# Performance work log

Measured on AMD Instinct MI355X. Metric: run time of the kernel, lower is better.

The kernel has to match this reference:

```python
import jax, jax.numpy as jnp
import numpy as np

NH = 8       # attention_maps
DK = 256     # key_dimension
DV = 256     # value_dimension
KS = 3       # kernel_size
PAD = (KS - 1) // 2


def _conv(x, w, b, stride, pad):
    y = jax.lax.conv_general_dilated(
        x, w, (stride, stride), [(pad, pad), (pad, pad)],
        dimension_numbers=('NCHW', 'OIHW', 'NCHW'))
    return y + b[None, :, None, None]


def _rel_to_abs(x):
    # x: (B, M, L, 2L-1) -> (B, M, L, L) via the skewing/padding trick
    B, M, L, _ = x.shape
    x = jnp.pad(x, ((0, 0), (0, 0), (0, 0), (0, 1)))          # (B,M,L,2L)
    x = x.reshape(B, M, 2 * L * L)
    x = jnp.pad(x, ((0, 0), (0, 0), (0, L - 1)))
    x = x.reshape(B, M, L + 1, 2 * L - 1)
    return x[:, :, :L, L - 1:]


def _rel_logits_1d(q, kr, H, W, nh, axis):
    # q: (B, nh, H, W, dkh); kr: (2W-1, dkh)
    B = q.shape[0]
    rl = jnp.einsum('bhxyd,md->bhxym', q, kr)                 # (B,nh,H,W,2W-1)
    rl = rl.reshape(B, nh * H, W, 2 * W - 1)
    rl = _rel_to_abs(rl).reshape(B, nh, H, W, W)
    rl = jnp.broadcast_to(rl[:, :, :, None], (B, nh, H, H, W, W))
    if axis == 'x':
        rl = jnp.transpose(rl, (0, 1, 2, 4, 3, 5))
    else:
        # faithful to original torch code (incl. its no-op transpose bug):
        # transpose(4,5) then transpose(3,5) == permutation (0,1,2,4,5,3)
        rl = jnp.transpose(rl, (0, 1, 2, 4, 5, 3))
    return rl.reshape(B, nh, H * W, H * W)


def setup_inputs() -> dict:
    key = jax.random.key(0)
    ks = jax.random.split(key, 10)
    B, Cin, H, W = 4, 128, 32, 32
    Cout = 512
    dkh = DK // NH
    sc = 0.05
    return {
        'x': jax.random.normal(ks[0], (B, Cin, H, W), jnp.float32),
        'conv_w': jax.random.normal(ks[1], (Cout - DV, Cin, KS, KS), jnp.float32) * sc,
        'conv_b': jax.random.normal(ks[2], (Cout - DV,), jnp.float32) * sc,
        'qkv_w': jax.random.normal(ks[3], (2 * DK + DV, Cin, KS, KS), jnp.float32) * sc,
        'qkv_b': jax.random.normal(ks[4], (2 * DK + DV,), jnp.float32) * sc,
        'att_w': jax.random.normal(ks[5], (DV, DV, 1, 1), jnp.float32) * sc,
        'att_b': jax.random.normal(ks[6], (DV,), jnp.float32) * sc,
        'kr_x': jax.random.normal(ks[7], (2 * W - 1, dkh), jnp.float32),
        'kr_y': jax.random.normal(ks[8], (2 * H - 1, dkh), jnp.float32),
    }


def reference(x, conv_w, conv_b, qkv_w, qkv_b, att_w, att_b, kr_x, kr_y):
    B = x.shape[0]
    conv_out = _conv(x, conv_w, conv_b, 1, PAD)               # (B, Cout-DV, H, W)
    H, W = conv_out.shape[2], conv_out.shape[3]
    dkh, dvh = DK // NH, DV // NH

    qkv = _conv(x, qkv_w, qkv_b, 1, PAD)                      # (B, 2DK+DV, H, W)
    q, k, v = jnp.split(qkv, [DK, 2 * DK], axis=1)
    q = q.reshape(B, NH, dkh, H, W) * (dkh ** -0.5)
    k = k.reshape(B, NH, dkh, H, W)
    v = v.reshape(B, NH, dvh, H, W)

    fq = q.reshape(B, NH, dkh, H * W)
    fk = k.reshape(B, NH, dkh, H * W)
    fv = v.reshape(B, NH, dvh, H * W)

    logits = jnp.einsum('bhdi,bhdj->bhij', fq, fk)            # (B,NH,HW,HW)

    # relative logits (scaled q, matching torch which scales before this)
    q_t = jnp.transpose(q, (0, 1, 3, 4, 2))                   # (B,NH,H,W,dkh)
    rel_x = _rel_logits_1d(q_t, kr_x, H, W, NH, 'x')
    rel_y = _rel_logits_1d(jnp.transpose(q_t, (0, 1, 3, 2, 4)), kr_y, W, H, NH, 'y')
    logits = logits + rel_y + rel_x

    weights = jax.nn.softmax(logits, axis=-1)
    att = jnp.einsum('bhij,bhdj->bhid', weights, fv)          # (B,NH,HW,dvh)
    # faithful raw reshape as in torch (no transpose before reshape)
    att = att.reshape(B, NH, dvh, H, W).reshape(B, DV, H, W)
    att = _conv(att, att_w, att_b, 1, 0)
    return jnp.concatenate([conv_out, att], axis=1)
```

## Files before the change

kernel.cpp:

```cpp
#include <hip/hip_runtime.h>
#include <hip/hip_bf16.h>
#include <math.h>

#define BN 4
#define CIN 128
#define HH 32
#define WW 32
#define HWP 1024
#define NHEAD 8

typedef __attribute__((ext_vector_type(8))) short s8v;
typedef __attribute__((ext_vector_type(4))) float f32x4;

__global__ __launch_bounds__(256) void prep_all(
    const float* __restrict__ x,
    const float* __restrict__ conv_w, const float* __restrict__ qkv_w,
    const float* __restrict__ att_w,
    const float* __restrict__ kr_x, const float* __restrict__ kr_y,
    __hip_bfloat16* __restrict__ xT, __hip_bfloat16* __restrict__ Wb,
    __hip_bfloat16* __restrict__ Wab, __hip_bfloat16* __restrict__ krb)
{
    const int bid = blockIdx.x;
    const int tid = threadIdx.x;

    if (bid < 4608) {
        int g = bid * 256 + tid;
        int co = g / 1152;
        int k = g - co * 1152;
        int kk = k >> 7, ci = k & 127;
        float v;
        if (co < 256) v = conv_w[((size_t)(co * 128 + ci) * 9) + kk];
        else          v = qkv_w[((size_t)((co - 256) * 128 + ci) * 9) + kk];
        Wb[(size_t)co * 1152 + k] = __float2bfloat16(v);
    } else if (bid < 4744) {
        __shared__ float xs[CIN][33];
        int rel = bid - 4608;
        int yy = rel >> 2;
        int b = rel & 3;
        const bool inner = (yy >= 1 && yy <= 32);
        if (inner) {
            for (int idx = tid; idx < CIN * 32; idx += 256) {
                int ci = idx >> 5, xx = idx & 31;
                xs[ci][xx] = x[((size_t)(b * CIN + ci) * HH + (yy - 1)) * WW + xx];
            }
        }
        __syncthreads();
        for (int idx = tid; idx < 34 * 128; idx += 256) {
            int xx = idx >> 7, ci = idx & 127;
            float v = 0.f;
            if (inner && xx >= 1 && xx <= 32) v = xs[ci][xx - 1];
            xT[((size_t)(b * 34 + yy) * 34 + xx) * 128 + ci] = __float2bfloat16(v);
        }
    } else if (bid < 5000) {
        int g = (bid - 4744) * 256 + tid;
        Wab[g] = __float2bfloat16(att_w[g]);
    } else {
        for (int idx = tid; idx < 2 * 64 * 32; idx += 256) {
            int axis = idx >> 11;
            int col = (idx >> 5) & 63;
            int d = idx & 31;
            float v = 0.f;
            if (col < 63) v = axis ? kr_y[col * 32 + d] : kr_x[col * 32 + d];
            krb[idx] = __float2bfloat16(v);
        }
    }
}

__global__ __launch_bounds__(256) void conv_gemm(
    const __hip_bfloat16* __restrict__ Wb, const __hip_bfloat16* __restrict__ xT,
    const float* __restrict__ conv_b, const float* __restrict__ qkv_b,
    float* __restrict__ out,
    __hip_bfloat16* __restrict__ qbf, __hip_bfloat16* __restrict__ kbf,
    __hip_bfloat16* __restrict__ vtb)
{
    __shared__ __align__(16) __hip_bfloat16 As[128 * 128];
    __shared__ __align__(16) __hip_bfloat16 Bs[128 * 128];

    const int tid = threadIdx.x;
    const int wv = tid >> 6;
    const int lane = tid & 63;
    const int n16 = lane & 15;
    const int quad = lane >> 4;
    const int co0 = blockIdx.x * 128;
    const int y0 = blockIdx.y * 4;
    const int b = blockIdx.z;
    const int mh = wv >> 1, nh = wv & 1;

    const int rbase = tid >> 4;
    const int hh = tid & 15;
    const int swz = (hh ^ rbase) * 8;
    const __hip_bfloat16* aGbase = Wb + (size_t)(co0 + rbase) * 1152 + hh * 8;

    f32x4 acc[4][4];
#pragma unroll
    for (int i = 0; i < 4; ++i)
#pragma unroll
        for (int j = 0; j < 4; ++j) acc[i][j] = (f32x4){0.f, 0.f, 0.f, 0.f};

    s8v ra[8], rb[8];

    auto load_tile = [&](int kk, s8v* la, s8v* lb) {
        const int ky = kk / 3, kx = kk - ky * 3;
#pragma unroll
        for (int i = 0; i < 8; ++i)
            la[i] = *reinterpret_cast<const s8v*>(aGbase + (size_t)(16 * i) * 1152 + kk * 128);
#pragma unroll
        for (int i = 0; i < 8; ++i) {
            int p = rbase + 16 * i;
            int row = y0 + (p >> 5) + ky;
            int xx = (p & 31) + kx;
            lb[i] = *reinterpret_cast<const s8v*>(
                xT + ((size_t)(b * 34 + row) * 34 + xx) * 128 + hh * 8);
        }
    };

    load_tile(0, ra, rb);

    for (int s = 0; s < 9; ++s) {
        __syncthreads();
#pragma unroll
        for (int i = 0; i < 8; ++i) {
            *reinterpret_cast<s8v*>(&As[(rbase + 16 * i) * 128 + swz]) = ra[i];
            *reinterpret_cast<s8v*>(&Bs[(rbase + 16 * i) * 128 + swz]) = rb[i];
        }
        __syncthreads();
        if (s < 8) load_tile(s + 1, ra, rb);

#pragma unroll
        for (int ksub = 0; ksub < 4; ++ksub) {
            const int chunk = ((ksub * 4 + quad) ^ n16) * 8;
            s8v af[4], bfr[4];
#pragma unroll
            for (int mt = 0; mt < 4; ++mt)
                af[mt] = *reinterpret_cast<const s8v*>(&As[(mh * 64 + mt * 16 + n16) * 128 + chunk]);
#pragma unroll
            for (int nt = 0; nt < 4; ++nt)
                bfr[nt] = *reinterpret_cast<const s8v*>(&Bs[(nh * 64 + nt * 16 + n16) * 128 + chunk]);
#pragma unroll
            for (int mt = 0; mt < 4; ++mt)
#pragma unroll
                for (int nt = 0; nt < 4; ++nt)
                    acc[mt][nt] = __builtin_amdgcn_mfma_f32_16x16x32_bf16(af[mt], bfr[nt], acc[mt][nt], 0, 0, 0);
        }
    }

    const int coBase = co0 + mh * 64;
    const int pixBase = y0 * 32 + nh * 64;
    const int seg = coBase >> 8;

    if (seg == 0) {
#pragma unroll
        for (int mt = 0; mt < 4; ++mt)
#pragma unroll
            for (int r = 0; r < 4; ++r) {
                int co = coBase + mt * 16 + quad * 4 + r;
                float bias = conv_b[co];
                float* op = out + (size_t)(b * 512 + co) * HWP + pixBase;
#pragma unroll
                for (int nt = 0; nt < 4; ++nt)
                    op[nt * 16 + n16] = acc[mt][nt][r] + bias;
            }
    } else if (seg == 1) {
        const float scale = 0.17677669529663687f;
#pragma unroll
        for (int mt = 0; mt < 4; ++mt)
#pragma unroll
            for (int r = 0; r < 4; ++r) {
                int c2 = coBase - 256 + mt * 16 + quad * 4 + r;
                float bias = qkv_b[c2];
                int h = c2 >> 5, d = c2 & 31;
                int bh = b * NHEAD + h;
#pragma unroll
                for (int nt = 0; nt < 4; ++nt) {
                    int pix = pixBase + nt * 16 + n16;
                    qbf[((size_t)bh * HWP + pix) * 32 + d] =
                        __float2bfloat16((acc[mt][nt][r] + bias) * scale);
                }
            }
    } else if (seg == 2) {
#pragma unroll
        for (int mt = 0; mt < 4; ++mt)
#pragma unroll
            for (int r = 0; r < 4; ++r) {
                int c2 = coBase - 512 + mt * 16 + quad * 4 + r;
                float bias = qkv_b[c2 + 256];
                int h = c2 >> 5, d = c2 & 31;
                int bh = b * NHEAD + h;
#pragma unroll
                for (int nt = 0; nt < 4; ++nt) {
                    int pix = pixBase + nt * 16 + n16;
                    kbf[((size_t)bh * HWP + pix) * 32 + d] =
                        __float2bfloat16(acc[mt][nt][r] + bias);
                }
            }
    } else {
#pragma unroll
        for (int mt = 0; mt < 4; ++mt)
#pragma unroll
            for (int r = 0; r < 4; ++r) {
                int c2 = coBase - 768 + mt * 16 + quad * 4 + r;
                float bias = qkv_b[c2 + 512];
                int h = c2 >> 5, d = c2 & 31;
                int bh = b * NHEAD + h;
                __hip_bfloat16* vp = vtb + ((size_t)bh * 32 + d) * HWP + pixBase;
#pragma unroll
                for (int nt = 0; nt < 4; ++nt)
                    vp[nt * 16 + n16] = __float2bfloat16(acc[mt][nt][r] + bias);
            }
    }
}

__global__ __launch_bounds__(256) void attn_kernel(
    const __hip_bfloat16* __restrict__ qbf, const __hip_bfloat16* __restrict__ kbf,
    const __hip_bfloat16* __restrict__ vtb, const __hip_bfloat16* __restrict__ krb,
    __hip_bfloat16* __restrict__ attc)
{
    __shared__ __align__(16) float QrX[4][16][68];
    __shared__ __align__(16) float QrY[4][16][68];
    __shared__ __align__(16) __hip_bfloat16 Pb[4][16][40];

    const int tid = threadIdx.x;
    const int wv = tid >> 6;
    const int lane = tid & 63;
    const int n16 = lane & 15;
    const int quad = lane >> 4;
    const int bh = blockIdx.x;
    const int i0 = (blockIdx.y * 4 + wv) * 16;
    const int xi0 = i0 & 31;
    const int yi0 = i0 >> 5;

    s8v aq = *reinterpret_cast<const s8v*>(
        qbf + ((size_t)bh * HWP + i0 + n16) * 32 + quad * 8);
    s8v aqT = *reinterpret_cast<const s8v*>(
        qbf + ((size_t)bh * HWP + (xi0 + n16) * 32 + yi0) * 32 + quad * 8);

#pragma unroll
    for (int t = 0; t < 4; ++t) {
        s8v bx = *reinterpret_cast<const s8v*>(krb + ((size_t)(t * 16 + n16)) * 32 + quad * 8);
        s8v by = *reinterpret_cast<const s8v*>(krb + ((size_t)(64 + t * 16 + n16)) * 32 + quad * 8);
        f32x4 cx = {0.f, 0.f, 0.f, 0.f}, cy = {0.f, 0.f, 0.f, 0.f};
        cx = __builtin_amdgcn_mfma_f32_16x16x32_bf16(aq, bx, cx, 0, 0, 0);
        cy = __builtin_amdgcn_mfma_f32_16x16x32_bf16(aqT, by, cy, 0, 0, 0);
#pragma unroll
        for (int r = 0; r < 4; ++r) {
            QrX[wv][quad * 4 + r][t * 16 + n16] = cx[r];
            QrY[wv][quad * 4 + r][t * 16 + n16] = cy[r];
        }
    }

    float rx0[4], rx1[4];
    int rybase[4];
#pragma unroll
    for (int r = 0; r < 4; ++r) {
        int xi = xi0 + quad * 4 + r;
        rx0[r] = QrX[wv][quad * 4 + r][n16 + 31 - xi];
        rx1[r] = QrX[wv][quad * 4 + r][n16 + 47 - xi];
        rybase[r] = 31 - xi;
    }

    float lsum[4] = {0.f, 0.f, 0.f, 0.f};
    f32x4 O0 = {0.f, 0.f, 0.f, 0.f}, O1 = {0.f, 0.f, 0.f, 0.f};

    const __hip_bfloat16* kbase = kbf + (size_t)bh * HWP * 32;
    const __hip_bfloat16* vbase = vtb + (size_t)bh * 32 * HWP;

    s8v bk0 = *reinterpret_cast<const s8v*>(kbase + ((size_t)n16 * 32 + quad * 8));
    s8v bk1 = *reinterpret_cast<const s8v*>(kbase + ((size_t)(16 + n16) * 32 + quad * 8));
    s8v bv0 = *reinterpret_cast<const s8v*>(vbase + ((size_t)n16 * HWP + quad * 8));
    s8v bv1 = *reinterpret_cast<const s8v*>(vbase + ((size_t)(n16 + 16) * HWP + quad * 8));

    for (int jt = 0; jt < 32; ++jt) {
        s8v cbk0 = bk0, cbk1 = bk1, cbv0 = bv0, cbv1 = bv1;
        if (jt < 31) {
            const int jn = (jt + 1) * 32;
            bk0 = *reinterpret_cast<const s8v*>(kbase + ((size_t)(jn + n16) * 32 + quad * 8));
            bk1 = *reinterpret_cast<const s8v*>(kbase + ((size_t)(jn + 16 + n16) * 32 + quad * 8));
            bv0 = *reinterpret_cast<const s8v*>(vbase + ((size_t)n16 * HWP + jn + quad * 8));
            bv1 = *reinterpret_cast<const s8v*>(vbase + ((size_t)(n16 + 16) * HWP + jn + quad * 8));
        }

        f32x4 s0 = {0.f, 0.f, 0.f, 0.f}, s1 = {0.f, 0.f, 0.f, 0.f};
        s0 = __builtin_amdgcn_mfma_f32_16x16x32_bf16(aq, cbk0, s0, 0, 0, 0);
        s1 = __builtin_amdgcn_mfma_f32_16x16x32_bf16(aq, cbk1, s1, 0, 0, 0);

#pragma unroll
        for (int r = 0; r < 4; ++r) {
            float ryv = QrY[wv][quad * 4 + r][jt + rybase[r]];
            float p0 = __expf(s0[r] + rx0[r] + ryv);
            float p1 = __expf(s1[r] + rx1[r] + ryv);
            lsum[r] += p0 + p1;
            Pb[wv][quad * 4 + r][n16]      = __float2bfloat16(p0);
            Pb[wv][quad * 4 + r][n16 + 16] = __float2bfloat16(p1);
        }
        s8v pA = *reinterpret_cast<const s8v*>(&Pb[wv][n16][quad * 8]);
        O0 = __builtin_amdgcn_mfma_f32_16x16x32_bf16(pA, cbv0, O0, 0, 0, 0);
        O1 = __builtin_amdgcn_mfma_f32_16x16x32_bf16(pA, cbv1, O1, 0, 0, 0);
    }

    const int b = bh >> 3, h = bh & 7;
#pragma unroll
    for (int r = 0; r < 4; ++r) {
        float l = lsum[r];
        l += __shfl_xor(l, 1);
        l += __shfl_xor(l, 2);
        l += __shfl_xor(l, 4);
        l += __shfl_xor(l, 8);
        float inv = 1.0f / l;
        int i = i0 + quad * 4 + r;
        int yi = i >> 5, xi = i & 31;
        __hip_bfloat16* op = attc + ((size_t)(b * 256 + h * 32 + yi) * 32 + xi) * 32;
        op[n16] = __float2bfloat16(O0[r] * inv);
        op[n16 + 16] = __float2bfloat16(O1[r] * inv);
    }
}

__global__ __launch_bounds__(256) void conv1x1_gemm(
    const __hip_bfloat16* __restrict__ Wab, const __hip_bfloat16* __restrict__ attc,
    const float* __restrict__ att_b, float* __restrict__ out)
{
    __shared__ __align__(16) __hip_bfloat16 Ls[64][264];

    const int tid = threadIdx.x;
    const int wv = tid >> 6;
    const int lane = tid & 63;
    const int n16 = lane & 15;
    const int quad = lane >> 4;
    const int o0 = blockIdx.x * 64;
    const int p0 = blockIdx.y * 64;
    const int b = blockIdx.z;
    const int oW = o0 + (wv >> 1) * 32;
    const int pL = (wv & 1) * 32;

#pragma unroll
    for (int pass = 0; pass < 8; ++pass) {
        int ch = pass * 32 + (tid >> 3);
        int pg = (tid & 7) * 8;
        s8v v = *reinterpret_cast<const s8v*>(
            attc + ((size_t)(b * 256 + ch) * HWP) + p0 + pg);
#pragma unroll
        for (int j = 0; j < 8; ++j)
            Ls[pg + j][ch] = ((const __hip_bfloat16*)&v)[j];
    }
    __syncthreads();

    f32x4 acc[2][2];
#pragma unroll
    for (int i = 0; i < 2; ++i)
#pragma unroll
        for (int j = 0; j < 2; ++j) acc[i][j] = (f32x4){0.f, 0.f, 0.f, 0.f};

#pragma unroll
    for (int ks = 0; ks < 8; ++ks) {
        const int c0 = ks * 32 + quad * 8;
        s8v a0 = *reinterpret_cast<const s8v*>(Wab + (size_t)(oW + n16) * 256 + c0);
        s8v a1 = *reinterpret_cast<const s8v*>(Wab + (size_t)(oW + 16 + n16) * 256 + c0);
        s8v b0 = *reinterpret_cast<const s8v*>(&Ls[pL + n16][c0]);
        s8v b1 = *reinterpret_cast<const s8v*>(&Ls[pL + 16 + n16][c0]);
        acc[0][0] = __builtin_amdgcn_mfma_f32_16x16x32_bf16(a0, b0, acc[0][0], 0, 0, 0);
        acc[0][1] = __builtin_amdgcn_mfma_f32_16x16x32_bf16(a0, b1, acc[0][1], 0, 0, 0);
        acc[1][0] = __builtin_amdgcn_mfma_f32_16x16x32_bf16(a1, b0, acc[1][0], 0, 0, 0);
        acc[1][1] = __builtin_amdgcn_mfma_f32_16x16x32_bf16(a1, b1, acc[1][1], 0, 0, 0);
    }

#pragma unroll
    for (int mt = 0; mt < 2; ++mt)
#pragma unroll
        for (int r = 0; r < 4; ++r) {
            int o = oW + mt * 16 + quad * 4 + r;
            float bias = att_b[o];
            float* op = out + ((size_t)(b * 512 + 256 + o)) * HWP;
#pragma unroll
            for (int nt = 0; nt < 2; ++nt)
                op[p0 + pL + nt * 16 + n16] = acc[mt][nt][r] + bias;
        }
}

extern "C" void kernel_launch(void* const* d_in, const int* in_sizes, int n_in,
                              void* d_out, int out_size, void* d_ws, size_t ws_size,
                              hipStream_t stream) {
    const float* x      = (const float*)d_in[0];
    const float* conv_w = (const float*)d_in[1];
    const float* conv_b = (const float*)d_in[2];
    const float* qkv_w  = (const float*)d_in[3];
    const float* qkv_b  = (const float*)d_in[4];
    const float* att_w  = (const float*)d_in[5];
    const float* att_b  = (const float*)d_in[6];
    const float* kr_x   = (const float*)d_in[7];
    const float* kr_y   = (const float*)d_in[8];
    float* out = (float*)d_out;

    char* base = (char*)d_ws;
    const size_t MB = 1u << 20;
    __hip_bfloat16* qbf  = (__hip_bfloat16*)(base + 0 * MB);
    __hip_bfloat16* kbf  = (__hip_bfloat16*)(base + 2 * MB);
    __hip_bfloat16* vtb  = (__hip_bfloat16*)(base + 4 * MB);
    __hip_bfloat16* xT   = (__hip_bfloat16*)(base + 6 * MB);
    __hip_bfloat16* Wb   = (__hip_bfloat16*)(base + 8 * MB);
    __hip_bfloat16* attc = (__hip_bfloat16*)(base + 11 * MB);
    __hip_bfloat16* Wab  = (__hip_bfloat16*)(base + 13 * MB);
    __hip_bfloat16* krb  = (__hip_bfloat16*)(base + 14 * MB);

    prep_all<<<dim3(5001), 256, 0, stream>>>(
        x, conv_w, qkv_w, att_w, kr_x, kr_y, xT, Wb, Wab, krb);
    conv_gemm<<<dim3(8, 8, 4), 256, 0, stream>>>(
        Wb, xT, conv_b, qkv_b, out, qbf, kbf, vtb);
    attn_kernel<<<dim3(32, 16), 256, 0, stream>>>(qbf, kbf, vtb, krb, attc);
    conv1x1_gemm<<<dim3(4, 16, 4), 256, 0, stream>>>(Wab, attc, att_b, out);
}
```

Measured before the change: 140.1 us.

## Split attention key range across two wave groups with LDS reduction

Doubles the attention block to 512 threads so that each 16-row query tile is handled by two waves, each covering half of the key/value sequence. The upper waves write their partial output accumulators and row sums into shared memory, and after a barrier the lower waves add them in, normalize and store. This shortens the serial key loop per wave and raises the number of waves in flight. In exchange it adds shared memory, one block-wide sync and duplicated relative-logit setup work in both waves.

```diff
diff --git a/kernel.cpp b/kernel.cpp
--- a/kernel.cpp
+++ b/kernel.cpp
@@ -210,22 +210,25 @@
     }
 }
 
-__global__ __launch_bounds__(256) void attn_kernel(
+__global__ __launch_bounds__(512, 4) void attn_kernel(
     const __hip_bfloat16* __restrict__ qbf, const __hip_bfloat16* __restrict__ kbf,
     const __hip_bfloat16* __restrict__ vtb, const __hip_bfloat16* __restrict__ krb,
     __hip_bfloat16* __restrict__ attc)
 {
     __shared__ __align__(16) float QrX[4][16][68];
     __shared__ __align__(16) float QrY[4][16][68];
-    __shared__ __align__(16) __hip_bfloat16 Pb[4][16][40];
+    __shared__ __align__(16) __hip_bfloat16 Pb[8][16][40];
+    __shared__ float Ored[4][64][13];
 
     const int tid = threadIdx.x;
     const int wv = tid >> 6;
     const int lane = tid & 63;
     const int n16 = lane & 15;
     const int quad = lane >> 4;
+    const int itl = wv & 3;
+    const int jh = wv >> 2;
     const int bh = blockIdx.x;
-    const int i0 = (blockIdx.y * 4 + wv) * 16;
+    const int i0 = (blockIdx.y * 4 + itl) * 16;
     const int xi0 = i0 & 31;
     const int yi0 = i0 >> 5;
 
@@ -243,8 +246,8 @@
         cy = __builtin_amdgcn_mfma_f32_16x16x32_bf16(aqT, by, cy, 0, 0, 0);
 #pragma unroll
         for (int r = 0; r < 4; ++r) {
-            QrX[wv][quad * 4 + r][t * 16 + n16] = cx[r];
-            QrY[wv][quad * 4 + r][t * 16 + n16] = cy[r];
+            QrX[itl][quad * 4 + r][t * 16 + n16] = cx[r];
+            QrY[itl][quad * 4 + r][t * 16 + n16] = cy[r];
         }
     }
 
@@ -253,8 +256,8 @@
 #pragma unroll
     for (int r = 0; r < 4; ++r) {
         int xi = xi0 + quad * 4 + r;
-        rx0[r] = QrX[wv][quad * 4 + r][n16 + 31 - xi];
-        rx1[r] = QrX[wv][quad * 4 + r][n16 + 47 - xi];
+        rx0[r] = QrX[itl][quad * 4 + r][n16 + 31 - xi];
+        rx1[r] = QrX[itl][quad * 4 + r][n16 + 47 - xi];
         rybase[r] = 31 - xi;
     }
 
@@ -264,53 +267,77 @@
     const __hip_bfloat16* kbase = kbf + (size_t)bh * HWP * 32;
     const __hip_bfloat16* vbase = vtb + (size_t)bh * 32 * HWP;
 
-    s8v bk0 = *reinterpret_cast<const s8v*>(kbase + ((size_t)n16 * 32 + quad * 8));
-    s8v bk1 = *reinterpret_cast<const s8v*>(kbase + ((size_t)(16 + n16) * 32 + quad * 8));
-    s8v bv0 = *reinterpret_cast<const s8v*>(vbase + ((size_t)n16 * HWP + quad * 8));
-    s8v bv1 = *reinterpret_cast<const s8v*>(vbase + ((size_t)(n16 + 16) * HWP + quad * 8));
-
-    for (int jt = 0; jt < 32; ++jt) {
-        s8v cbk0 = bk0, cbk1 = bk1, cbv0 = bv0, cbv1 = bv1;
-        if (jt < 31) {
-            const int jn = (jt + 1) * 32;
-            bk0 = *reinterpret_cast<const s8v*>(kbase + ((size_t)(jn + n16) * 32 + quad * 8));
-            bk1 = *reinterpret_cast<const s8v*>(kbase + ((size_t)(jn + 16 + n16) * 32 + quad * 8));
-            bv0 = *reinterpret_cast<const s8v*>(vbase + ((size_t)n16 * HWP + jn + quad * 8));
-            bv1 = *reinterpret_cast<const s8v*>(vbase + ((size_t)(n16 + 16) * HWP + jn + quad * 8));
-        }
-
-        f32x4 s0 = {0.f, 0.f, 0.f, 0.f}, s1 = {0.f, 0.f, 0.f, 0.f};
-        s0 = __builtin_amdgcn_mfma_f32_16x16x32_bf16(aq, cbk0, s0, 0, 0, 0);
-        s1 = __builtin_amdgcn_mfma_f32_16x16x32_bf16(aq, cbk1, s1, 0, 0, 0);
-
+    const int jbeg = jh * 16;
+    {
+        const int j0 = jbeg * 32;
+        s8v bk0 = *reinterpret_cast<const s8v*>(kbase + ((size_t)(j0 + n16) * 32 + quad * 8));
+        s8v bk1 = *reinterpret_cast<const s8v*>(kbase + ((size_t)(j0 + 16 + n16) * 32 + quad * 8));
+        s8v bv0 = *reinterpret_cast<const s8v*>(vbase + ((size_t)n16 * HWP + j0 + quad * 8));
+        s8v bv1 = *reinterpret_cast<const s8v*>(vbase + ((size_t)(n16 + 16) * HWP + j0 + quad * 8));
+
+        for (int t = 0; t < 16; ++t) {
+            const int jt = jbeg + t;
+            s8v cbk0 = bk0, cbk1 = bk1, cbv0 = bv0, cbv1 = bv1;
+            if (t < 15) {
+                const int jn = (jt + 1) * 32;
+                bk0 = *reinterpret_cast<const s8v*>(kbase + ((size_t)(jn + n16) * 32 + quad * 8));
+                bk1 = *reinterpret_cast<const s8v*>(kbase + ((size_t)(jn + 16 + n16) * 32 + quad * 8));
+                bv0 = *reinterpret_cast<const s8v*>(vbase + ((size_t)n16 * HWP + jn + quad * 8));
+                bv1 = *reinterpret_cast<const s8v*>(vbase + ((size_t)(n16 + 16) * HWP + jn + quad * 8));
+            }
+
+            f32x4 s0 = {0.f, 0.f, 0.f, 0.f}, s1 = {0.f, 0.f, 0.f, 0.f};
+            s0 = __builtin_amdgcn_mfma_f32_16x16x32_bf16(aq, cbk0, s0, 0, 0, 0);
+            s1 = __builtin_amdgcn_mfma_f32_16x16x32_bf16(aq, cbk1, s1, 0, 0, 0);
+
+#pragma unroll
+            for (int r = 0; r < 4; ++r) {
+                float ryv = QrY[itl][quad * 4 + r][jt + rybase[r]];
+                float p0 = __expf(s0[r] + rx0[r] + ryv);
+                float p1 = __expf(s1[r] + rx1[r] + ryv);
+                lsum[r] += p0 + p1;
+                Pb[wv][quad * 4 + r][n16]      = __float2bfloat16(p0);
+                Pb[wv][quad * 4 + r][n16 + 16] = __float2bfloat16(p1);
+            }
+            s8v pA = *reinterpret_cast<const s8v*>(&Pb[wv][n16][quad * 8]);
+            O0 = __builtin_amdgcn_mfma_f32_16x16x32_bf16(pA, cbv0, O0, 0, 0, 0);
+            O1 = __builtin_amdgcn_mfma_f32_16x16x32_bf16(pA, cbv1, O1, 0, 0, 0);
+        }
+    }
+
+    if (wv >= 4) {
+        float* dst = &Ored[itl][lane][0];
 #pragma unroll
         for (int r = 0; r < 4; ++r) {
-            float ryv = QrY[wv][quad * 4 + r][jt + rybase[r]];
-            float p0 = __expf(s0[r] + rx0[r] + ryv);
-            float p1 = __expf(s1[r] + rx1[r] + ryv);
-            lsum[r] += p0 + p1;
-            Pb[wv][quad * 4 + r][n16]      = __float2bfloat16(p0);
-            Pb[wv][quad * 4 + r][n16 + 16] = __float2bfloat16(p1);
-        }
-        s8v pA = *reinterpret_cast<const s8v*>(&Pb[wv][n16][quad * 8]);
-        O0 = __builtin_amdgcn_mfma_f32_16x16x32_bf16(pA, cbv0, O0, 0, 0, 0);
-        O1 = __builtin_amdgcn_mfma_f32_16x16x32_bf16(pA, cbv1, O1, 0, 0, 0);
-    }
-
-    const int b = bh >> 3, h = bh & 7;
-#pragma unroll
-    for (int r = 0; r < 4; ++r) {
-        float l = lsum[r];
-        l += __shfl_xor(l, 1);
-        l += __shfl_xor(l, 2);
-        l += __shfl_xor(l, 4);
-        l += __shfl_xor(l, 8);
-        float inv = 1.0f / l;
-        int i = i0 + quad * 4 + r;
-        int yi = i >> 5, xi = i & 31;
-        __hip_bfloat16* op = attc + ((size_t)(b * 256 + h * 32 + yi) * 32 + xi) * 32;
-        op[n16] = __float2bfloat16(O0[r] * inv);
-        op[n16 + 16] = __float2bfloat16(O1[r] * inv);
+            dst[r] = O0[r];
+            dst[4 + r] = O1[r];
+            dst[8 + r] = lsum[r];
+        }
+    }
+    __syncthreads();
+    if (wv < 4) {
+        const float* src = &Ored[itl][lane][0];
+#pragma unroll
+        for (int r = 0; r < 4; ++r) {
+            O0[r] += src[r];
+            O1[r] += src[4 + r];
+            lsum[r] += src[8 + r];
+        }
+        const int b = bh >> 3, h = bh & 7;
+#pragma unroll
+        for (int r = 0; r < 4; ++r) {
+            float l = lsum[r];
+            l += __shfl_xor(l, 1);
+            l += __shfl_xor(l, 2);
+            l += __shfl_xor(l, 4);
+            l += __shfl_xor(l, 8);
+            float inv = 1.0f / l;
+            int i = i0 + quad * 4 + r;
+            int yi = i >> 5, xi = i & 31;
+            __hip_bfloat16* op = attc + ((size_t)(b * 256 + h * 32 + yi) * 32 + xi) * 32;
+            op[n16] = __float2bfloat16(O0[r] * inv);
+            op[n16 + 16] = __float2bfloat16(O1[r] * inv);
+        }
     }
 }
 
@@ -404,6 +431,6 @@
         x, conv_w, qkv_w, att_w, kr_x, kr_y, xT, Wb, Wab, krb);
     conv_gemm<<<dim3(8, 8, 4), 256, 0, stream>>>(
         Wb, xT, conv_b, qkv_b, out, qbf, kbf, vtb);
-    attn_kernel<<<dim3(32, 16), 256, 0, stream>>>(qbf, kbf, vtb, krb, attc);
+    attn_kernel<<<dim3(32, 16), 512, 0, stream>>>(qbf, kbf, vtb, krb, attc);
     conv1x1_gemm<<<dim3(4, 16, 4), 256, 0, stream>>>(Wab, attc, att_b, out);
 }
```

Result: no change. 142.2 us (+1.5%).

## Fuse all four stages into one persistent kernel with grid barriers

Applied to the files above, without the earlier changes.

Replaces the four separate launches (prep, conv GEMM, attention, 1x1 conv) with a single persistent kernel of 512 blocks. The stages are separated by atomic-counter grid barriers, and a memset resets the counters before the launch. The aim is to remove launch gaps and tail effects between stages. To fit the fixed grid, the conv GEMM and 1x1 tiles are halved, the prep work becomes a grid-stride loop, and the xT transpose no longer goes through shared memory. This relies on all 512 blocks being co-resident (launch bounds allow 2 per CU) to avoid deadlock, and the smaller tiles reduce data reuse.

```diff
diff --git a/kernel.cpp b/kernel.cpp
--- a/kernel.cpp
+++ b/kernel.cpp
@@ -2,377 +2,367 @@
 #include <hip/hip_bf16.h>
 #include <math.h>
 
-#define BN 4
-#define CIN 128
-#define HH 32
-#define WW 32
 #define HWP 1024
 #define NHEAD 8
+#define NBLK 512
 
 typedef __attribute__((ext_vector_type(8))) short s8v;
 typedef __attribute__((ext_vector_type(4))) float f32x4;
 
-__global__ __launch_bounds__(256) void prep_all(
+#define WB_N   1179648
+#define XT_N   591872
+#define WAB_N  65536
+#define KRB_N  4096
+#define TOT_PREP (WB_N + XT_N + WAB_N + KRB_N)
+
+__device__ __forceinline__ void grid_barrier(unsigned* cnt) {
+    __syncthreads();
+    if (threadIdx.x == 0) {
+        __threadfence();
+        atomicAdd(cnt, 1u);
+        while (atomicAdd(cnt, 0u) < NBLK) __builtin_amdgcn_s_sleep(2);
+        __threadfence();
+    }
+    __syncthreads();
+}
+
+__global__ __launch_bounds__(256, 2) void mega_kernel(
     const float* __restrict__ x,
-    const float* __restrict__ conv_w, const float* __restrict__ qkv_w,
-    const float* __restrict__ att_w,
+    const float* __restrict__ conv_w, const float* __restrict__ conv_b,
+    const float* __restrict__ qkv_w, const float* __restrict__ qkv_b,
+    const float* __restrict__ att_w, const float* __restrict__ att_b,
     const float* __restrict__ kr_x, const float* __restrict__ kr_y,
-    __hip_bfloat16* __restrict__ xT, __hip_bfloat16* __restrict__ Wb,
-    __hip_bfloat16* __restrict__ Wab, __hip_bfloat16* __restrict__ krb)
-{
-    const int bid = blockIdx.x;
-    const int tid = threadIdx.x;
-
-    if (bid < 4608) {
-        int g = bid * 256 + tid;
-        int co = g / 1152;
-        int k = g - co * 1152;
-        int kk = k >> 7, ci = k & 127;
-        float v;
-        if (co < 256) v = conv_w[((size_t)(co * 128 + ci) * 9) + kk];
-        else          v = qkv_w[((size_t)((co - 256) * 128 + ci) * 9) + kk];
-        Wb[(size_t)co * 1152 + k] = __float2bfloat16(v);
-    } else if (bid < 4744) {
-        __shared__ float xs[CIN][33];
-        int rel = bid - 4608;
-        int yy = rel >> 2;
-        int b = rel & 3;
-        const bool inner = (yy >= 1 && yy <= 32);
-        if (inner) {
-            for (int idx = tid; idx < CIN * 32; idx += 256) {
-                int ci = idx >> 5, xx = idx & 31;
-                xs[ci][xx] = x[((size_t)(b * CIN + ci) * HH + (yy - 1)) * WW + xx];
-            }
-        }
-        __syncthreads();
-        for (int idx = tid; idx < 34 * 128; idx += 256) {
-            int xx = idx >> 7, ci = idx & 127;
-            float v = 0.f;
-            if (inner && xx >= 1 && xx <= 32) v = xs[ci][xx - 1];
-            xT[((size_t)(b * 34 + yy) * 34 + xx) * 128 + ci] = __float2bfloat16(v);
-        }
-    } else if (bid < 5000) {
-        int g = (bid - 4744) * 256 + tid;
-        Wab[g] = __float2bfloat16(att_w[g]);
-    } else {
-        for (int idx = tid; idx < 2 * 64 * 32; idx += 256) {
-            int axis = idx >> 11;
-            int col = (idx >> 5) & 63;
-            int d = idx & 31;
-            float v = 0.f;
-            if (col < 63) v = axis ? kr_y[col * 32 + d] : kr_x[col * 32 + d];
-            krb[idx] = __float2bfloat16(v);
-        }
-    }
-}
-
-__global__ __launch_bounds__(256) void conv_gemm(
-    const __hip_bfloat16* __restrict__ Wb, const __hip_bfloat16* __restrict__ xT,
-    const float* __restrict__ conv_b, const float* __restrict__ qkv_b,
     float* __restrict__ out,
     __hip_bfloat16* __restrict__ qbf, __hip_bfloat16* __restrict__ kbf,
-    __hip_bfloat16* __restrict__ vtb)
+    __hip_bfloat16* __restrict__ vtb, __hip_bfloat16* __restrict__ xT,
+    __hip_bfloat16* __restrict__ Wb, __hip_bfloat16* __restrict__ Wab,
+    __hip_bfloat16* __restrict__ krb, __hip_bfloat16* __restrict__ attc,
+    unsigned* __restrict__ bar)
 {
-    __shared__ __align__(16) __hip_bfloat16 As[128 * 128];
-    __shared__ __align__(16) __hip_bfloat16 Bs[128 * 128];
-
+    __shared__ __align__(16) char smem[49152];
+
+    const int bid = blockIdx.x;
     const int tid = threadIdx.x;
     const int wv = tid >> 6;
     const int lane = tid & 63;
     const int n16 = lane & 15;
     const int quad = lane >> 4;
-    const int co0 = blockIdx.x * 128;
-    const int y0 = blockIdx.y * 4;
-    const int b = blockIdx.z;
-    const int mh = wv >> 1, nh = wv & 1;
-
-    const int rbase = tid >> 4;
-    const int hh = tid & 15;
-    const int swz = (hh ^ rbase) * 8;
-    const __hip_bfloat16* aGbase = Wb + (size_t)(co0 + rbase) * 1152 + hh * 8;
-
-    f32x4 acc[4][4];
-#pragma unroll
-    for (int i = 0; i < 4; ++i)
-#pragma unroll
-        for (int j = 0; j < 4; ++j) acc[i][j] = (f32x4){0.f, 0.f, 0.f, 0.f};
-
-    s8v ra[8], rb[8];
-
-    auto load_tile = [&](int kk, s8v* la, s8v* lb) {
-        const int ky = kk / 3, kx = kk - ky * 3;
-#pragma unroll
-        for (int i = 0; i < 8; ++i)
-            la[i] = *reinterpret_cast<const s8v*>(aGbase + (size_t)(16 * i) * 1152 + kk * 128);
-#pragma unroll
-        for (int i = 0; i < 8; ++i) {
-            int p = rbase + 16 * i;
-            int row = y0 + (p >> 5) + ky;
-            int xx = (p & 31) + kx;
-            lb[i] = *reinterpret_cast<const s8v*>(
-                xT + ((size_t)(b * 34 + row) * 34 + xx) * 128 + hh * 8);
-        }
-    };
-
-    load_tile(0, ra, rb);
-
-    for (int s = 0; s < 9; ++s) {
+
+    {
+        for (int g = bid * 256 + tid; g < TOT_PREP; g += NBLK * 256) {
+            if (g < WB_N) {
+                int co = g / 1152;
+                int k = g - co * 1152;
+                int kk = k >> 7, ci = k & 127;
+                float v;
+                if (co < 256) v = conv_w[((size_t)(co * 128 + ci) * 9) + kk];
+                else          v = qkv_w[((size_t)((co - 256) * 128 + ci) * 9) + kk];
+                Wb[(size_t)co * 1152 + k] = __float2bfloat16(v);
+            } else if (g < WB_N + XT_N) {
+                int rel = g - WB_N;
+                int ci = rel & 127;
+                int t = rel >> 7;
+                int xx = t % 34;
+                int t2 = t / 34;
+                int yy = t2 % 34;
+                int b = t2 / 34;
+                float v = 0.f;
+                int gy = yy - 1, gx = xx - 1;
+                if ((unsigned)gy < 32u && (unsigned)gx < 32u)
+                    v = x[((size_t)(b * 128 + ci) * 32 + gy) * 32 + gx];
+                xT[(size_t)rel] = __float2bfloat16(v);
+            } else if (g < WB_N + XT_N + WAB_N) {
+                int rel = g - (WB_N + XT_N);
+                Wab[rel] = __float2bfloat16(att_w[rel]);
+            } else {
+                int rel = g - (WB_N + XT_N + WAB_N);
+                int col = (rel >> 5) & 63;
+                int d = rel & 31;
+                int axis = rel >> 11;
+                float v = 0.f;
+                if (col < 63) v = axis ? kr_y[col * 32 + d] : kr_x[col * 32 + d];
+                krb[rel] = __float2bfloat16(v);
+            }
+        }
+    }
+    grid_barrier(&bar[0]);
+
+    {
+        __hip_bfloat16* As = (__hip_bfloat16*)smem;
+        __hip_bfloat16* Bs = (__hip_bfloat16*)(smem + 32768);
+        const int ph = bid & 1;
+        const int b = (bid >> 1) & 3;
+        const int yt = (bid >> 3) & 7;
+        const int ct = bid >> 6;
+        const int co0 = ct * 128;
+        const int pixBase = yt * 128 + ph * 64;
+        const int row0 = pixBase >> 5;
+        const int mh = wv >> 1, nh = wv & 1;
+        const int rbase = tid >> 4;
+        const int hh = tid & 15;
+        const int swz = (hh ^ rbase) * 8;
+        const __hip_bfloat16* aGbase = Wb + (size_t)(co0 + rbase) * 1152 + hh * 8;
+
+        f32x4 acc[4][2];
+#pragma unroll
+        for (int i = 0; i < 4; ++i)
+#pragma unroll
+            for (int j = 0; j < 2; ++j) acc[i][j] = (f32x4){0.f, 0.f, 0.f, 0.f};
+
+        s8v ra[8], rb2[4];
+        auto load_tile = [&](int kk, s8v* la, s8v* lb) {
+            const int ky = kk / 3, kx = kk - ky * 3;
+#pragma unroll
+            for (int i = 0; i < 8; ++i)
+                la[i] = *reinterpret_cast<const s8v*>(aGbase + (size_t)(16 * i) * 1152 + kk * 128);
+#pragma unroll
+            for (int i = 0; i < 4; ++i) {
+                int p = rbase + 16 * i;
+                lb[i] = *reinterpret_cast<const s8v*>(
+                    xT + ((size_t)(b * 34 + row0 + (p >> 5) + ky) * 34 + (p & 31) + kx) * 128 + hh * 8);
+            }
+        };
+
+        load_tile(0, ra, rb2);
+
+        for (int s = 0; s < 9; ++s) {
+            __syncthreads();
+#pragma unroll
+            for (int i = 0; i < 8; ++i)
+                *reinterpret_cast<s8v*>(&As[(rbase + 16 * i) * 128 + swz]) = ra[i];
+#pragma unroll
+            for (int i = 0; i < 4; ++i)
+                *reinterpret_cast<s8v*>(&Bs[(rbase + 16 * i) * 128 + swz]) = rb2[i];
+            __syncthreads();
+            if (s < 8) load_tile(s + 1, ra, rb2);
+
+#pragma unroll
+            for (int ksub = 0; ksub < 4; ++ksub) {
+                const int chunk = ((ksub * 4 + quad) ^ n16) * 8;
+                s8v af[4], bfr[2];
+#pragma unroll
+                for (int mt = 0; mt < 4; ++mt)
+                    af[mt] = *reinterpret_cast<const s8v*>(&As[(mh * 64 + mt * 16 + n16) * 128 + chunk]);
+#pragma unroll
+                for (int nt = 0; nt < 2; ++nt)
+                    bfr[nt] = *reinterpret_cast<const s8v*>(&Bs[(nh * 32 + nt * 16 + n16) * 128 + chunk]);
+#pragma unroll
+                for (int mt = 0; mt < 4; ++mt)
+#pragma unroll
+                    for (int nt = 0; nt < 2; ++nt)
+                        acc[mt][nt] = __builtin_amdgcn_mfma_f32_16x16x32_bf16(af[mt], bfr[nt], acc[mt][nt], 0, 0, 0);
+            }
+        }
+
+        const int coBase = co0 + mh * 64;
+        const int pixW = pixBase + nh * 32;
+        const int seg = coBase >> 8;
+
+        if (seg == 0) {
+#pragma unroll
+            for (int mt = 0; mt < 4; ++mt)
+#pragma unroll
+                for (int r = 0; r < 4; ++r) {
+                    int co = coBase + mt * 16 + quad * 4 + r;
+                    float bias = conv_b[co];
+                    float* op = out + (size_t)(b * 512 + co) * HWP + pixW;
+#pragma unroll
+                    for (int nt = 0; nt < 2; ++nt)
+                        op[nt * 16 + n16] = acc[mt][nt][r] + bias;
+                }
+        } else if (seg == 1) {
+            const float scale = 0.17677669529663687f;
+#pragma unroll
+            for (int mt = 0; mt < 4; ++mt)
+#pragma unroll
+                for (int r = 0; r < 4; ++r) {
+                    int c2 = coBase - 256 + mt * 16 + quad * 4 + r;
+                    float bias = qkv_b[c2];
+                    int h = c2 >> 5, d = c2 & 31;
+                    int bh = b * NHEAD + h;
+#pragma unroll
+                    for (int nt = 0; nt < 2; ++nt) {
+                        int pix = pixW + nt * 16 + n16;
+                        qbf[((size_t)bh * HWP + pix) * 32 + d] =
+                            __float2bfloat16((acc[mt][nt][r] + bias) * scale);
+                    }
+                }
+        } else if (seg == 2) {
+#pragma unroll
+            for (int mt = 0; mt < 4; ++mt)
+#pragma unroll
+                for (int r = 0; r < 4; ++r) {
+                    int c2 = coBase - 512 + mt * 16 + quad * 4 + r;
+                    float bias = qkv_b[c2 + 256];
+                    int h = c2 >> 5, d = c2 & 31;
+                    int bh = b * NHEAD + h;
+#pragma unroll
+                    for (int nt = 0; nt < 2; ++nt) {
+                        int pix = pixW + nt * 16 + n16;
+                        kbf[((size_t)bh * HWP + pix) * 32 + d] =
+                            __float2bfloat16(acc[mt][nt][r] + bias);
+                    }
+                }
+        } else {
+#pragma unroll
+            for (int mt = 0; mt < 4; ++mt)
+#pragma unroll
+                for (int r = 0; r < 4; ++r) {
+                    int c2 = coBase - 768 + mt * 16 + quad * 4 + r;
+                    float bias = qkv_b[c2 + 512];
+                    int h = c2 >> 5, d = c2 & 31;
+                    int bh = b * NHEAD + h;
+                    __hip_bfloat16* vp = vtb + ((size_t)bh * 32 + d) * HWP + pixW;
+#pragma unroll
+                    for (int nt = 0; nt < 2; ++nt)
+                        vp[nt * 16 + n16] = __float2bfloat16(acc[mt][nt][r] + bias);
+                }
+        }
+    }
+    grid_barrier(&bar[32]);
+
+    {
+        float* QrX = (float*)smem;
+        float* QrY = (float*)(smem + 17408);
+        __hip_bfloat16* Pb = (__hip_bfloat16*)(smem + 34816);
+
+        const int bh = bid & 31;
+        const int iblk = bid >> 5;
+        const int i0 = (iblk * 4 + wv) * 16;
+        const int xi0 = i0 & 31;
+        const int yi0 = i0 >> 5;
+
+        s8v aq = *reinterpret_cast<const s8v*>(
+            qbf + ((size_t)bh * HWP + i0 + n16) * 32 + quad * 8);
+        s8v aqT = *reinterpret_cast<const s8v*>(
+            qbf + ((size_t)bh * HWP + (xi0 + n16) * 32 + yi0) * 32 + quad * 8);
+
+#pragma unroll
+        for (int t = 0; t < 4; ++t) {
+            s8v bx = *reinterpret_cast<const s8v*>(krb + ((size_t)(t * 16 + n16)) * 32 + quad * 8);
+            s8v by = *reinterpret_cast<const s8v*>(krb + ((size_t)(64 + t * 16 + n16)) * 32 + quad * 8);
+            f32x4 cx = {0.f, 0.f, 0.f, 0.f}, cy = {0.f, 0.f, 0.f, 0.f};
+            cx = __builtin_amdgcn_mfma_f32_16x16x32_bf16(aq, bx, cx, 0, 0, 0);
+            cy = __builtin_amdgcn_mfma_f32_16x16x32_bf16(aqT, by, cy, 0, 0, 0);
+#pragma unroll
+            for (int r = 0; r < 4; ++r) {
+                QrX[(wv * 16 + quad * 4 + r) * 68 + t * 16 + n16] = cx[r];
+                QrY[(wv * 16 + quad * 4 + r) * 68 + t * 16 + n16] = cy[r];
+            }
+        }
+
+        float rx0[4], rx1[4];
+        int rybase[4];
+#pragma unroll
+        for (int r = 0; r < 4; ++r) {
+            int xi = xi0 + quad * 4 + r;
+            rx0[r] = QrX[(wv * 16 + quad * 4 + r) * 68 + n16 + 31 - xi];
+            rx1[r] = QrX[(wv * 16 + quad * 4 + r) * 68 + n16 + 47 - xi];
+            rybase[r] = 31 - xi;
+        }
+
+        float lsum[4] = {0.f, 0.f, 0.f, 0.f};
+        f32x4 O0 = {0.f, 0.f, 0.f, 0.f}, O1 = {0.f, 0.f, 0.f, 0.f};
+
+        const __hip_bfloat16* kbase = kbf + (size_t)bh * HWP * 32;
+        const __hip_bfloat16* vbase = vtb + (size_t)bh * 32 * HWP;
+
+        s8v bk0 = *reinterpret_cast<const s8v*>(kbase + ((size_t)n16 * 32 + quad * 8));
+        s8v bk1 = *reinterpret_cast<const s8v*>(kbase + ((size_t)(16 + n16) * 32 + quad * 8));
+        s8v bv0 = *reinterpret_cast<const s8v*>(vbase + ((size_t)n16 * HWP + quad * 8));
+        s8v bv1 = *reinterpret_cast<const s8v*>(vbase + ((size_t)(n16 + 16) * HWP + quad * 8));
+
+        for (int jt = 0; jt < 32; ++jt) {
+            s8v cbk0 = bk0, cbk1 = bk1, cbv0 = bv0, cbv1 = bv1;
+            if (jt < 31) {
+                const int jn = (jt + 1) * 32;
+                bk0 = *reinterpret_cast<const s8v*>(kbase + ((size_t)(jn + n16) * 32 + quad * 8));
+                bk1 = *reinterpret_cast<const s8v*>(kbase + ((size_t)(jn + 16 + n16) * 32 + quad * 8));
+                bv0 = *reinterpret_cast<const s8v*>(vbase + ((size_t)n16 * HWP + jn + quad * 8));
+                bv1 = *reinterpret_cast<const s8v*>(vbase + ((size_t)(n16 + 16) * HWP + jn + quad * 8));
+            }
+
+            f32x4 s0 = {0.f, 0.f, 0.f, 0.f}, s1 = {0.f, 0.f, 0.f, 0.f};
+            s0 = __builtin_amdgcn_mfma_f32_16x16x32_bf16(aq, cbk0, s0, 0, 0, 0);
+            s1 = __builtin_amdgcn_mfma_f32_16x16x32_bf16(aq, cbk1, s1, 0, 0, 0);
+
+#pragma unroll
+            for (int r = 0; r < 4; ++r) {
+                float ryv = QrY[(wv * 16 + quad * 4 + r) * 68 + jt + rybase[r]];
+                float p0 = __expf(s0[r] + rx0[r] + ryv);
+                float p1 = __expf(s1[r] + rx1[r] + ryv);
+                lsum[r] += p0 + p1;
+                Pb[(wv * 16 + quad * 4 + r) * 40 + n16]      = __float2bfloat16(p0);
+                Pb[(wv * 16 + quad * 4 + r) * 40 + n16 + 16] = __float2bfloat16(p1);
+            }
+            s8v pA = *reinterpret_cast<const s8v*>(&Pb[(wv * 16 + n16) * 40 + quad * 8]);
+            O0 = __builtin_amdgcn_mfma_f32_16x16x32_bf16(pA, cbv0, O0, 0, 0, 0);
+            O1 = __builtin_amdgcn_mfma_f32_16x16x32_bf16(pA, cbv1, O1, 0, 0, 0);
+        }
+
+        const int b = bh >> 3, h = bh & 7;
+#pragma unroll
+        for (int r = 0; r < 4; ++r) {
+            float l = lsum[r];
+            l += __shfl_xor(l, 1);
+            l += __shfl_xor(l, 2);
+            l += __shfl_xor(l, 4);
+            l += __shfl_xor(l, 8);
+            float inv = 1.0f / l;
+            int i = i0 + quad * 4 + r;
+            int yi = i >> 5, xi = i & 31;
+            __hip_bfloat16* op = attc + ((size_t)(b * 256 + h * 32 + yi) * 32 + xi) * 32;
+            op[n16] = __float2bfloat16(O0[r] * inv);
+            op[n16 + 16] = __float2bfloat16(O1[r] * inv);
+        }
+    }
+    grid_barrier(&bar[64]);
+
+    {
+        __hip_bfloat16* Ls = (__hip_bfloat16*)smem;
+        const int o0 = (bid & 7) * 32;
+        const int pt = (bid >> 3) & 15;
+        const int b = bid >> 7;
+        const int p0 = pt * 64;
+        const int oW = o0 + (wv >> 1) * 16;
+        const int pL = (wv & 1) * 32;
+
+#pragma unroll
+        for (int pass = 0; pass < 8; ++pass) {
+            int ch = pass * 32 + (tid >> 3);
+            int pg = (tid & 7) * 8;
+            s8v v = *reinterpret_cast<const s8v*>(
+                attc + ((size_t)(b * 256 + ch) * HWP) + p0 + pg);
+#pragma unroll
+            for (int j = 0; j < 8; ++j)
+                Ls[(pg + j) * 264 + ch] = ((const __hip_bfloat16*)&v)[j];
+        }
         __syncthreads();
-#pragma unroll
-        for (int i = 0; i < 8; ++i) {
-            *reinterpret_cast<s8v*>(&As[(rbase + 16 * i) * 128 + swz]) = ra[i];
-            *reinterpret_cast<s8v*>(&Bs[(rbase + 16 * i) * 128 + swz]) = rb[i];
-        }
-        __syncthreads();
-        if (s < 8) load_tile(s + 1, ra, rb);
-
-#pragma unroll
-        for (int ksub = 0; ksub < 4; ++ksub) {
-            const int chunk = ((ksub * 4 + quad) ^ n16) * 8;
-            s8v af[4], bfr[4];
-#pragma unroll
-            for (int mt = 0; mt < 4; ++mt)
-                af[mt] = *reinterpret_cast<const s8v*>(&As[(mh * 64 + mt * 16 + n16) * 128 + chunk]);
-#pragma unroll
-            for (int nt = 0; nt < 4; ++nt)
-                bfr[nt] = *reinterpret_cast<const s8v*>(&Bs[(nh * 64 + nt * 16 + n16) * 128 + chunk]);
-#pragma unroll
-            for (int mt = 0; mt < 4; ++mt)
-#pragma unroll
-                for (int nt = 0; nt < 4; ++nt)
-                    acc[mt][nt] = __builtin_amdgcn_mfma_f32_16x16x32_bf16(af[mt], bfr[nt], acc[mt][nt], 0, 0, 0);
-        }
-    }
-
-    const int coBase = co0 + mh * 64;
-    const int pixBase = y0 * 32 + nh * 64;
-    const int seg = coBase >> 8;
-
-    if (seg == 0) {
-#pragma unroll
-        for (int mt = 0; mt < 4; ++mt)
-#pragma unroll
-            for (int r = 0; r < 4; ++r) {
-                int co = coBase + mt * 16 + quad * 4 + r;
-                float bias = conv_b[co];
-                float* op = out + (size_t)(b * 512 + co) * HWP + pixBase;
-#pragma unroll
-                for (int nt = 0; nt < 4; ++nt)
-                    op[nt * 16 + n16] = acc[mt][nt][r] + bias;
-            }
-    } else if (seg == 1) {
-        const float scale = 0.17677669529663687f;
-#pragma unroll
-        for (int mt = 0; mt < 4; ++mt)
-#pragma unroll
-            for (int r = 0; r < 4; ++r) {
-                int c2 = coBase - 256 + mt * 16 + quad * 4 + r;
-                float bias = qkv_b[c2];
-                int h = c2 >> 5, d = c2 & 31;
-                int bh = b * NHEAD + h;
-#pragma unroll
-                for (int nt = 0; nt < 4; ++nt) {
-                    int pix = pixBase + nt * 16 + n16;
-                    qbf[((size_t)bh * HWP + pix) * 32 + d] =
-                        __float2bfloat16((acc[mt][nt][r] + bias) * scale);
-                }
-            }
-    } else if (seg == 2) {
-#pragma unroll
-        for (int mt = 0; mt < 4; ++mt)
-#pragma unroll
-            for (int r = 0; r < 4; ++r) {
-                int c2 = coBase - 512 + mt * 16 + quad * 4 + r;
-                float bias = qkv_b[c2 + 256];
-                int h = c2 >> 5, d = c2 & 31;
-                int bh = b * NHEAD + h;
-#pragma unroll
-                for (int nt = 0; nt < 4; ++nt) {
-                    int pix = pixBase + nt * 16 + n16;
-                    kbf[((size_t)bh * HWP + pix) * 32 + d] =
-                        __float2bfloat16(acc[mt][nt][r] + bias);
-                }
-            }
-    } else {
-#pragma unroll
-        for (int mt = 0; mt < 4; ++mt)
-#pragma unroll
-            for (int r = 0; r < 4; ++r) {
-                int c2 = coBase - 768 + mt * 16 + quad * 4 + r;
-                float bias = qkv_b[c2 + 512];
-                int h = c2 >> 5, d = c2 & 31;
-                int bh = b * NHEAD + h;
-                __hip_bfloat16* vp = vtb + ((size_t)bh * 32 + d) * HWP + pixBase;
-#pragma unroll
-                for (int nt = 0; nt < 4; ++nt)
-                    vp[nt * 16 + n16] = __float2bfloat16(acc[mt][nt][r] + bias);
-            }
-    }
-}
-
-__global__ __launch_bounds__(256) void attn_kernel(
-    const __hip_bfloat16* __restrict__ qbf, const __hip_bfloat16* __restrict__ kbf,
-    const __hip_bfloat16* __restrict__ vtb, const __hip_bfloat16* __restrict__ krb,
-    __hip_bfloat16* __restrict__ attc)
-{
-    __shared__ __align__(16) float QrX[4][16][68];
-    __shared__ __align__(16) float QrY[4][16][68];
-    __shared__ __align__(16) __hip_bfloat16 Pb[4][16][40];
-
-    const int tid = threadIdx.x;
-    const int wv = tid >> 6;
-    const int lane = tid & 63;
-    const int n16 = lane & 15;
-    const int quad = lane >> 4;
-    const int bh = blockIdx.x;
-    const int i0 = (blockIdx.y * 4 + wv) * 16;
-    const int xi0 = i0 & 31;
-    const int yi0 = i0 >> 5;
-
-    s8v aq = *reinterpret_cast<const s8v*>(
-        qbf + ((size_t)bh * HWP + i0 + n16) * 32 + quad * 8);
-    s8v aqT = *reinterpret_cast<const s8v*>(
-        qbf + ((size_t)bh * HWP + (xi0 + n16) * 32 + yi0) * 32 + quad * 8);
-
-#pragma unroll
-    for (int t = 0; t < 4; ++t) {
-        s8v bx = *reinterpret_cast<const s8v*>(krb + ((size_t)(t * 16 + n16)) * 32 + quad * 8);
-        s8v by = *reinterpret_cast<const s8v*>(krb + ((size_t)(64 + t * 16 + n16)) * 32 + quad * 8);
-        f32x4 cx = {0.f, 0.f, 0.f, 0.f}, cy = {0.f, 0.f, 0.f, 0.f};
-        cx = __builtin_amdgcn_mfma_f32_16x16x32_bf16(aq, bx, cx, 0, 0, 0);
-        cy = __builtin_amdgcn_mfma_f32_16x16x32_bf16(aqT, by, cy, 0, 0, 0);
+
+        f32x4 acc[2];
+        acc[0] = (f32x4){0.f, 0.f, 0.f, 0.f};
+        acc[1] = (f32x4){0.f, 0.f, 0.f, 0.f};
+
+#pragma unroll
+        for (int ks = 0; ks < 8; ++ks) {
+            const int c0 = ks * 32 + quad * 8;
+            s8v a0 = *reinterpret_cast<const s8v*>(Wab + (size_t)(oW + n16) * 256 + c0);
+            s8v b0 = *reinterpret_cast<const s8v*>(&Ls[(pL + n16) * 264 + c0]);
+            s8v b1 = *reinterpret_cast<const s8v*>(&Ls[(pL + 16 + n16) * 264 + c0]);
+            acc[0] = __builtin_amdgcn_mfma_f32_16x16x32_bf16(a0, b0, acc[0], 0, 0, 0);
+            acc[1] = __builtin_amdgcn_mfma_f32_16x16x32_bf16(a0, b1, acc[1], 0, 0, 0);
+        }
+
 #pragma unroll
         for (int r = 0; r < 4; ++r) {
-            QrX[wv][quad * 4 + r][t * 16 + n16] = cx[r];
-            QrY[wv][quad * 4 + r][t * 16 + n16] = cy[r];
-        }
-    }
-
-    float rx0[4], rx1[4];
-    int rybase[4];
-#pragma unroll
-    for (int r = 0; r < 4; ++r) {
-        int xi = xi0 + quad * 4 + r;
-        rx0[r] = QrX[wv][quad * 4 + r][n16 + 31 - xi];
-        rx1[r] = QrX[wv][quad * 4 + r][n16 + 47 - xi];
-        rybase[r] = 31 - xi;
-    }
-
-    float lsum[4] = {0.f, 0.f, 0.f, 0.f};
-    f32x4 O0 = {0.f, 0.f, 0.f, 0.f}, O1 = {0.f, 0.f, 0.f, 0.f};
-
-    const __hip_bfloat16* kbase = kbf + (size_t)bh * HWP * 32;
-    const __hip_bfloat16* vbase = vtb + (size_t)bh * 32 * HWP;
-
-    s8v bk0 = *reinterpret_cast<const s8v*>(kbase + ((size_t)n16 * 32 + quad * 8));
-    s8v bk1 = *reinterpret_cast<const s8v*>(kbase + ((size_t)(16 + n16) * 32 + quad * 8));
-    s8v bv0 = *reinterpret_cast<const s8v*>(vbase + ((size_t)n16 * HWP + quad * 8));
-    s8v bv1 = *reinterpret_cast<const s8v*>(vbase + ((size_t)(n16 + 16) * HWP + quad * 8));
-
-    for (int jt = 0; jt < 32; ++jt) {
-        s8v cbk0 = bk0, cbk1 = bk1, cbv0 = bv0, cbv1 = bv1;
-        if (jt < 31) {
-            const int jn = (jt + 1) * 32;
-            bk0 = *reinterpret_cast<const s8v*>(kbase + ((size_t)(jn + n16) * 32 + quad * 8));
-            bk1 = *reinterpret_cast<const s8v*>(kbase + ((size_t)(jn + 16 + n16) * 32 + quad * 8));
-            bv0 = *reinterpret_cast<const s8v*>(vbase + ((size_t)n16 * HWP + jn + quad * 8));
-            bv1 = *reinterpret_cast<const s8v*>(vbase + ((size_t)(n16 + 16) * HWP + jn + quad * 8));
-        }
-
-        f32x4 s0 = {0.f, 0.f, 0.f, 0.f}, s1 = {0.f, 0.f, 0.f, 0.f};
-        s0 = __builtin_amdgcn_mfma_f32_16x16x32_bf16(aq, cbk0, s0, 0, 0, 0);
-        s1 = __builtin_amdgcn_mfma_f32_16x16x32_bf16(aq, cbk1, s1, 0, 0, 0);
-
-#pragma unroll
-        for (int r = 0; r < 4; ++r) {
-            float ryv = QrY[wv][quad * 4 + r][jt + rybase[r]];
-            float p0 = __expf(s0[r] + rx0[r] + ryv);
-            float p1 = __expf(s1[r] + rx1[r] + ryv);
-            lsum[r] += p0 + p1;
-            Pb[wv][quad * 4 + r][n16]      = __float2bfloat16(p0);
-            Pb[wv][quad * 4 + r][n16 + 16] = __float2bfloat16(p1);
-        }
-        s8v pA = *reinterpret_cast<const s8v*>(&Pb[wv][n16][quad * 8]);
-        O0 = __builtin_amdgcn_mfma_f32_16x16x32_bf16(pA, cbv0, O0, 0, 0, 0);
-        O1 = __builtin_amdgcn_mfma_f32_16x16x32_bf16(pA, cbv1, O1, 0, 0, 0);
-    }
-
-    const int b = bh >> 3, h = bh & 7;
-#pragma unroll
-    for (int r = 0; r < 4; ++r) {
-        float l = lsum[r];
-        l += __shfl_xor(l, 1);
-        l += __shfl_xor(l, 2);
-        l += __shfl_xor(l, 4);
-        l += __shfl_xor(l, 8);
-        float inv = 1.0f / l;
-        int i = i0 + quad * 4 + r;
-        int yi = i >> 5, xi = i & 31;
-        __hip_bfloat16* op = attc + ((size_t)(b * 256 + h * 32 + yi) * 32 + xi) * 32;
-        op[n16] = __float2bfloat16(O0[r] * inv);
-        op[n16 + 16] = __float2bfloat16(O1[r] * inv);
-    }
-}
-
-__global__ __launch_bounds__(256) void conv1x1_gemm(
-    const __hip_bfloat16* __restrict__ Wab, const __hip_bfloat16* __restrict__ attc,
-    const float* __restrict__ att_b, float* __restrict__ out)
-{
-    __shared__ __align__(16) __hip_bfloat16 Ls[64][264];
-
-    const int tid = threadIdx.x;
-    const int wv = tid >> 6;
-    const int lane = tid & 63;
-    const int n16 = lane & 15;
-    const int quad = lane >> 4;
-    const int o0 = blockIdx.x * 64;
-    const int p0 = blockIdx.y * 64;
-    const int b = blockIdx.z;
-    const int oW = o0 + (wv >> 1) * 32;
-    const int pL = (wv & 1) * 32;
-
-#pragma unroll
-    for (int pass = 0; pass < 8; ++pass) {
-        int ch = pass * 32 + (tid >> 3);
-        int pg = (tid & 7) * 8;
-        s8v v = *reinterpret_cast<const s8v*>(
-            attc + ((size_t)(b * 256 + ch) * HWP) + p0 + pg);
-#pragma unroll
-        for (int j = 0; j < 8; ++j)
-            Ls[pg + j][ch] = ((const __hip_bfloat16*)&v)[j];
-    }
-    __syncthreads();
-
-    f32x4 acc[2][2];
-#pragma unroll
-    for (int i = 0; i < 2; ++i)
-#pragma unroll
-        for (int j = 0; j < 2; ++j) acc[i][j] = (f32x4){0.f, 0.f, 0.f, 0.f};
-
-#pragma unroll
-    for (int ks = 0; ks < 8; ++ks) {
-        const int c0 = ks * 32 + quad * 8;
-        s8v a0 = *reinterpret_cast<const s8v*>(Wab + (size_t)(oW + n16) * 256 + c0);
-        s8v a1 = *reinterpret_cast<const s8v*>(Wab + (size_t)(oW + 16 + n16) * 256 + c0);
-        s8v b0 = *reinterpret_cast<const s8v*>(&Ls[pL + n16][c0]);
-        s8v b1 = *reinterpret_cast<const s8v*>(&Ls[pL + 16 + n16][c0]);
-        acc[0][0] = __builtin_amdgcn_mfma_f32_16x16x32_bf16(a0, b0, acc[0][0], 0, 0, 0);
-        acc[0][1] = __builtin_amdgcn_mfma_f32_16x16x32_bf16(a0, b1, acc[0][1], 0, 0, 0);
-        acc[1][0] = __builtin_amdgcn_mfma_f32_16x16x32_bf16(a1, b0, acc[1][0], 0, 0, 0);
-        acc[1][1] = __builtin_amdgcn_mfma_f32_16x16x32_bf16(a1, b1, acc[1][1], 0, 0, 0);
-    }
-
-#pragma unroll
-    for (int mt = 0; mt < 2; ++mt)
-#pragma unroll
-        for (int r = 0; r < 4; ++r) {
-            int o = oW + mt * 16 + quad * 4 + r;
+            int o = oW + quad * 4 + r;
             float bias = att_b[o];
             float* op = out + ((size_t)(b * 512 + 256 + o)) * HWP;
 #pragma unroll
             for (int nt = 0; nt < 2; ++nt)
-                op[p0 + pL + nt * 16 + n16] = acc[mt][nt][r] + bias;
-        }
+                op[p0 + pL + nt * 16 + n16] = acc[nt][r] + bias;
+        }
+    }
 }
 
 extern "C" void kernel_launch(void* const* d_in, const int* in_sizes, int n_in,
@@ -399,11 +389,10 @@
     __hip_bfloat16* attc = (__hip_bfloat16*)(base + 11 * MB);
     __hip_bfloat16* Wab  = (__hip_bfloat16*)(base + 13 * MB);
     __hip_bfloat16* krb  = (__hip_bfloat16*)(base + 14 * MB);
-
-    prep_all<<<dim3(5001), 256, 0, stream>>>(
-        x, conv_w, qkv_w, att_w, kr_x, kr_y, xT, Wb, Wab, krb);
-    conv_gemm<<<dim3(8, 8, 4), 256, 0, stream>>>(
-        Wb, xT, conv_b, qkv_b, out, qbf, kbf, vtb);
-    attn_kernel<<<dim3(32, 16), 256, 0, stream>>>(qbf, kbf, vtb, krb, attc);
-    conv1x1_gemm<<<dim3(4, 16, 4), 256, 0, stream>>>(Wab, attc, att_b, out);
+    unsigned* bar        = (unsigned*)(base + 15 * MB);
+
+    hipMemsetAsync(bar, 0, 384, stream);
+    mega_kernel<<<dim3(NBLK), 256, 0, stream>>>(
+        x, conv_w, conv_b, qkv_w, qkv_b, att_w, att_b, kr_x, kr_y, out,
+        qbf, kbf, vtb, xT, Wb, Wab, krb, attc, bar);
 }
```

Result: slower. 299.7 us (+113.9%).
